# Performance work log

Measured on AMD Instinct MI355X. Metric: run time of the kernel, lower is better.

## Reference

```python
import jax, jax.numpy as jnp
import numpy as np

DZ, DA, K, T, BS, H = 32, 16, 3, 128, 512, 128


def setup_inputs() -> dict:
    key = jax.random.key(0)
    ks = jax.random.split(key, 8)
    s = 0.02
    # A/C: identity-like init (as in the torch module) plus small noise, per mixture k and timestep t
    A = jnp.eye(DZ, dtype=jnp.float32) + s * jax.random.normal(ks[0], (K, T, DZ, DZ), jnp.float32)
    C = jnp.eye(DA, DZ, dtype=jnp.float32) + s * jax.random.normal(ks[1], (K, T, DA, DZ), jnp.float32)
    a0 = jnp.zeros((DA,), jnp.float32)
    a = jax.random.normal(ks[2], (BS, T, DA), jnp.float32)

    def lw(k, shape):
        return 0.05 * jax.random.normal(k, shape, jnp.float32)

    Wih0 = lw(ks[3], (4 * H, DA)); Whh0 = lw(ks[4], (4 * H, H))
    bih0 = jnp.zeros((4 * H,), jnp.float32); bhh0 = jnp.zeros((4 * H,), jnp.float32)
    Wih1 = lw(ks[5], (4 * H, H)); Whh1 = lw(ks[6], (4 * H, H))
    bih1 = jnp.zeros((4 * H,), jnp.float32); bhh1 = jnp.zeros((4 * H,), jnp.float32)
    Wlin = lw(ks[7], (K, H)); blin = jnp.zeros((K,), jnp.float32)
    return dict(a=a, A=A, C=C, a0=a0, Wih0=Wih0, Whh0=Whh0, bih0=bih0, bhh0=bhh0,
                Wih1=Wih1, Whh1=Whh1, bih1=bih1, bhh1=bhh1, Wlin=Wlin, blin=blin)


def _lstm_layer(x, Wih, Whh, bih, bhh):
    # x: (bs, L, din) -> (bs, L, H); PyTorch gate order i, f, g, o; zero initial state
    Hd = Whh.shape[1]
    b = bih + bhh

    def step(carry, xt):
        h, c = carry
        g = xt @ Wih.T + h @ Whh.T + b
        i, f, gg, o = jnp.split(g, 4, axis=-1)
        c = jax.nn.sigmoid(f) * c + jax.nn.sigmoid(i) * jnp.tanh(gg)
        h = jax.nn.sigmoid(o) * jnp.tanh(c)
        return (h, c), h

    h0 = jnp.zeros((x.shape[0], Hd), x.dtype)
    _, hs = jax.lax.scan(step, (h0, h0), jnp.swapaxes(x, 0, 1))
    return jnp.swapaxes(hs, 0, 1)


def _filter(a, A, C, a0, Wih0, Whh0, bih0, bhh0, Wih1, Whh1, bih1, bhh1, Wlin, blin):
    bs, L, da = a.shape
    dz = A.shape[-1]
    R = 0.01 * jnp.eye(da, dtype=a.dtype)
    Q = 0.01 * jnp.eye(dz, dtype=a.dtype)

    # dynamics network: alpha_t from [a_0, a_0..a_{L-2}]
    code = jnp.concatenate([jnp.broadcast_to(a0, (bs, 1, da)), a[:, :-1]], axis=1)
    h = _lstm_layer(code, Wih0, Whh0, bih0, bhh0)
    h = _lstm_layer(h, Wih1, Whh1, bih1, bhh1)
    alpha = jax.nn.softmax(h @ Wlin.T + blin, axis=-1)  # (bs, L, K)

    A_mix = jnp.einsum('blk,klij->blij', alpha, A)  # (bs, L, dz, dz)
    C_mix = jnp.einsum('blk,klij->blij', alpha, C)  # (bs, L, da, dz)
    # A is applied at index t+1 for the prediction step; last slot is a dummy (its output is unused)
    A_next = jnp.concatenate([A_mix[:, 1:], A_mix[:, -1:]], axis=1)

    mu0 = jnp.zeros((bs, dz), a.dtype)
    sig0 = jnp.broadcast_to(jnp.eye(dz, dtype=a.dtype), (bs, dz, dz))
    I = jnp.eye(dz, dtype=a.dtype)

    def step(carry, inp):
        mu_pred, sigma_pred = carry
        Ct, At_next, at = inp  # (bs,da,dz), (bs,dz,dz), (bs,da)
        r = at - jnp.einsum('bij,bj->bi', Ct, mu_pred)
        CtT = jnp.swapaxes(Ct, 1, 2)
        S = Ct @ sigma_pred @ CtT + R                      # (bs, da, da)
        Kg = sigma_pred @ CtT @ jnp.linalg.inv(S)          # (bs, dz, da)
        mu = mu_pred + jnp.einsum('bij,bj->bi', Kg, r)
        sigma = (I - Kg @ Ct) @ sigma_pred
        mu_next = jnp.einsum('bij,bj->bi', At_next, mu)
        sigma_next = At_next @ sigma @ jnp.swapaxes(At_next, 1, 2) + Q
        return (mu_next, sigma_next), mu

    xs = (jnp.swapaxes(C_mix, 0, 1), jnp.swapaxes(A_next, 0, 1), jnp.swapaxes(a, 0, 1))
    _, means = jax.lax.scan(step, (mu0, sig0), xs)
    return jnp.swapaxes(means, 0, 1)  # filtered means (bs, L, dz)


def reference(a, A, C, a0, Wih0, Whh0, bih0, bhh0, Wih1, Whh1, bih1, bhh1, Wlin, blin):
    return _filter(a, A, C, a0, Wih0, Whh0, bih0, bhh0,
                   Wih1, Whh1, bih1, bhh1, Wlin, blin)
```

## Files before the change

kernel.cpp:

```cpp
#include <hip/hip_runtime.h>
#include <hip/hip_fp16.h>
#include <cstdint>

#define T_LEN 128
#define DA    16
#define DZ    32
#define HH    128

__device__ __forceinline__ float sigm(float x){ return 1.0f/(1.0f + __expf(-x)); }
__device__ __forceinline__ float tanh_f(float x){ return 1.0f - 2.0f/(__expf(2.0f*x)+1.0f); }
__device__ __forceinline__ float dot4(float4 a, float4 b){ return a.x*b.x + a.y*b.y + a.z*b.z + a.w*b.w; }

typedef _Float16 h2v __attribute__((ext_vector_type(2)));
__device__ __forceinline__ float fdot2(uint32_t w, uint32_t h, float acc){
  union{uint32_t u; h2v v;} a, b; a.u = w; b.u = h;
  return __builtin_amdgcn_fdot2(a.v, b.v, acc, false);
}
__device__ __forceinline__ uint32_t packh2(float x, float y){
  return (uint32_t)__half_as_ushort(__float2half(x)) |
         ((uint32_t)__half_as_ushort(__float2half(y)) << 16);
}

#define BAR() do { asm volatile("s_waitcnt lgkmcnt(0)" ::: "memory"); \
                   __builtin_amdgcn_s_barrier(); } while (0)


__global__ void prep_kernel(const float* __restrict__ Wih0, const float* __restrict__ Whh0,
                            const float* __restrict__ bih0, const float* __restrict__ bhh0,
                            const float* __restrict__ Wih1, const float* __restrict__ Whh1,
                            const float* __restrict__ bih1, const float* __restrict__ bhh1,
                            uint32_t* __restrict__ ws) {
  int idx = blockIdx.x*256 + threadIdx.x;
  if (idx < 4096) {
    int q = idx & 3, g = (idx >> 2) & 511, m = idx >> 11;
    int k0 = 8*m + 2*q;
    ws[idx] = packh2(Wih0[g*DA + k0], Wih0[g*DA + k0 + 1]);
  } else if (idx < 36864) {
    int f = idx - 4096;
    int q = f & 3, g = (f >> 2) & 511, m = f >> 11;
    int k0 = 8*m + 2*q;
    ws[idx] = packh2(Whh0[g*HH + k0], Whh0[g*HH + k0 + 1]);
  } else if (idx < 69632) {
    int f = idx - 36864;
    int q = f & 3, g = (f >> 2) & 511, m = f >> 11;
    int k0 = 8*m + 2*q;
    ws[idx] = packh2(Wih1[g*HH + k0], Wih1[g*HH + k0 + 1]);
  } else if (idx < 102400) {
    int f = idx - 69632;
    int q = f & 3, g = (f >> 2) & 511, m = f >> 11;
    int k0 = 8*m + 2*q;
    ws[idx] = packh2(Whh1[g*HH + k0], Whh1[g*HH + k0 + 1]);
  } else if (idx < 102912) {
    int j = idx - 102400;
    ((float*)ws)[idx] = bih0[j] + bhh0[j];
  } else if (idx < 103424) {
    int j = idx - 102912;
    ((float*)ws)[idx] = bih1[j] + bhh1[j];
  }
}

__global__ __launch_bounds__(512, 2) void lstm_kernel(
    const float* __restrict__ a, const float* __restrict__ a0,
    const uint32_t* __restrict__ wsw, const float* __restrict__ Wlin,
    const float* __restrict__ blin, float* __restrict__ alpha_out) {
  const uint4* Wih0p = (const uint4*)(wsw);
  const uint4* Whh0p = (const uint4*)(wsw + 4096);
  const uint4* Wih1p = (const uint4*)(wsw + 36864);
  const uint4* Whh1p = (const uint4*)(wsw + 69632);
  const float* b0v = (const float*)(wsw + 102400);
  const float* b1v = (const float*)(wsw + 102912);

  __shared__ __align__(16) uint32_t sxh[2][T_LEN][8];
  __shared__ __align__(16) uint32_t sh0h[2][64];
  __shared__ __align__(16) uint32_t sh1h[2][64];
  __shared__ float gates[2][4*HH];

  int tid = threadIdx.x;
  int lane = tid & 63;
  int wv = tid >> 6;
  int bb = blockIdx.x * 2;

  uint4 wi0[2], wh0[16], wi1[16], wh1[16];
  #pragma unroll
  for (int m = 0; m < 2; ++m)  wi0[m] = Wih0p[m*512 + tid];
  #pragma unroll
  for (int m = 0; m < 16; ++m) wh0[m] = Whh0p[m*512 + tid];
  #pragma unroll
  for (int m = 0; m < 16; ++m) wi1[m] = Wih1p[m*512 + tid];
  #pragma unroll
  for (int m = 0; m < 16; ++m) wh1[m] = Whh1p[m*512 + tid];
  float bi0 = b0v[tid], bi1 = b1v[tid];

  for (int i = tid; i < 2*T_LEN*8; i += 512) {
    int r = i / (T_LEN*8), rem = i % (T_LEN*8), t = rem >> 3, p = rem & 7;
    float x0, x1;
    if (t == 0) { x0 = a0[2*p]; x1 = a0[2*p+1]; }
    else {
      const float* src = a + ((size_t)(bb + r)*T_LEN + (t-1))*DA;
      x0 = src[2*p]; x1 = src[2*p+1];
    }
    sxh[r][t][p] = packh2(x0, x1);
  }
  float wl00 = Wlin[0*HH + 2*lane], wl01 = Wlin[0*HH + 2*lane+1];
  float wl10 = Wlin[1*HH + 2*lane], wl11 = Wlin[1*HH + 2*lane+1];
  float wl20 = Wlin[2*HH + 2*lane], wl21 = Wlin[2*HH + 2*lane+1];
  float bl0 = blin[0], bl1 = blin[1], bl2 = blin[2];
  float c00 = 0.f, c01 = 0.f, c10 = 0.f, c11 = 0.f;
  if (tid < 128) { sh0h[wv][lane] = 0u; sh1h[wv][lane] = 0u; }
  __syncthreads();

  #pragma unroll 1
  for (int t = 0; t < T_LEN; ++t) {
    {
      float g0a = bi0, g0b = 0.f, g1a = bi0, g1b = 0.f;
      uint4 xA0 = *(const uint4*)&sxh[0][t][0];
      uint4 xA1 = *(const uint4*)&sxh[0][t][4];
      uint4 xB0 = *(const uint4*)&sxh[1][t][0];
      uint4 xB1 = *(const uint4*)&sxh[1][t][4];
      g0a = fdot2(wi0[0].x, xA0.x, g0a); g0b = fdot2(wi0[0].y, xA0.y, g0b);
      g0a = fdot2(wi0[0].z, xA0.z, g0a); g0b = fdot2(wi0[0].w, xA0.w, g0b);
      g0a = fdot2(wi0[1].x, xA1.x, g0a); g0b = fdot2(wi0[1].y, xA1.y, g0b);
      g0a = fdot2(wi0[1].z, xA1.z, g0a); g0b = fdot2(wi0[1].w, xA1.w, g0b);
      g1a = fdot2(wi0[0].x, xB0.x, g1a); g1b = fdot2(wi0[0].y, xB0.y, g1b);
      g1a = fdot2(wi0[0].z, xB0.z, g1a); g1b = fdot2(wi0[0].w, xB0.w, g1b);
      g1a = fdot2(wi0[1].x, xB1.x, g1a); g1b = fdot2(wi0[1].y, xB1.y, g1b);
      g1a = fdot2(wi0[1].z, xB1.z, g1a); g1b = fdot2(wi0[1].w, xB1.w, g1b);
      #pragma unroll
      for (int m = 0; m < 16; ++m) {
        uint4 w = wh0[m];
        uint4 hA = *(const uint4*)&sh0h[0][4*m];
        uint4 hB = *(const uint4*)&sh0h[1][4*m];
        g0a = fdot2(w.x, hA.x, g0a); g0b = fdot2(w.y, hA.y, g0b);
        g0a = fdot2(w.z, hA.z, g0a); g0b = fdot2(w.w, hA.w, g0b);
        g1a = fdot2(w.x, hB.x, g1a); g1b = fdot2(w.y, hB.y, g1b);
        g1a = fdot2(w.z, hB.z, g1a); g1b = fdot2(w.w, hB.w, g1b);
      }
      gates[0][tid] = g0a + g0b;
      gates[1][tid] = g1a + g1b;
    }
    __syncthreads();
    if (tid < 128) {
      int j0 = 2*lane, j1 = j0 + 1;
      float i0 = gates[wv][j0],      f0 = gates[wv][j0+HH],
            q0 = gates[wv][j0+2*HH], o0 = gates[wv][j0+3*HH];
      c00 = sigm(f0)*c00 + sigm(i0)*tanh_f(q0);
      float hv0 = sigm(o0)*tanh_f(c00);
      float i1 = gates[wv][j1],      f1 = gates[wv][j1+HH],
            q1 = gates[wv][j1+2*HH], o1 = gates[wv][j1+3*HH];
      c01 = sigm(f1)*c01 + sigm(i1)*tanh_f(q1);
      float hv1 = sigm(o1)*tanh_f(c01);
      sh0h[wv][lane] = packh2(hv0, hv1);
    }
    __syncthreads();
    {
      float g0a = bi1, g0b = 0.f, g1a = bi1, g1b = 0.f;
      #pragma unroll
      for (int m = 0; m < 16; ++m) {
        uint4 w = wi1[m];
        uint4 hA = *(const uint4*)&sh0h[0][4*m];
        uint4 hB = *(const uint4*)&sh0h[1][4*m];
        g0a = fdot2(w.x, hA.x, g0a); g0b = fdot2(w.y, hA.y, g0b);
        g0a = fdot2(w.z, hA.z, g0a); g0b = fdot2(w.w, hA.w, g0b);
        g1a = fdot2(w.x, hB.x, g1a); g1b = fdot2(w.y, hB.y, g1b);
        g1a = fdot2(w.z, hB.z, g1a); g1b = fdot2(w.w, hB.w, g1b);
      }
      #pragma unroll
      for (int m = 0; m < 16; ++m) {
        uint4 w = wh1[m];
        uint4 hA = *(const uint4*)&sh1h[0][4*m];
        uint4 hB = *(const uint4*)&sh1h[1][4*m];
        g0a = fdot2(w.x, hA.x, g0a); g0b = fdot2(w.y, hA.y, g0b);
        g0a = fdot2(w.z, hA.z, g0a); g0b = fdot2(w.w, hA.w, g0b);
        g1a = fdot2(w.x, hB.x, g1a); g1b = fdot2(w.y, hB.y, g1b);
        g1a = fdot2(w.w, hB.w, g1b); g1a = fdot2(w.z, hB.z, g1a);
      }
      gates[0][tid] = g0a + g0b;
      gates[1][tid] = g1a + g1b;
    }
    __syncthreads();
    float hv0 = 0.f, hv1 = 0.f;
    if (tid < 128) {
      int j0 = 2*lane, j1 = j0 + 1;
      float i0 = gates[wv][j0],      f0 = gates[wv][j0+HH],
            q0 = gates[wv][j0+2*HH], o0 = gates[wv][j0+3*HH];
      c10 = sigm(f0)*c10 + sigm(i0)*tanh_f(q0);
      hv0 = sigm(o0)*tanh_f(c10);
      float i1 = gates[wv][j1],      f1 = gates[wv][j1+HH],
            q1 = gates[wv][j1+2*HH], o1 = gates[wv][j1+3*HH];
      c11 = sigm(f1)*c11 + sigm(i1)*tanh_f(q1);
      hv1 = sigm(o1)*tanh_f(c11);
      sh1h[wv][lane] = packh2(hv0, hv1);
    }
    __syncthreads();
    if (tid < 128) {
      float p0 = hv0*wl00 + hv1*wl01;
      float p1 = hv0*wl10 + hv1*wl11;
      float p2 = hv0*wl20 + hv1*wl21;
      #pragma unroll
      for (int off = 32; off > 0; off >>= 1) {
        p0 += __shfl_down(p0, off); p1 += __shfl_down(p1, off); p2 += __shfl_down(p2, off);
      }
      if (lane == 0) {
        float l0 = p0 + bl0, l1 = p1 + bl1, l2 = p2 + bl2;
        float mx = fmaxf(l0, fmaxf(l1, l2));
        float e0=__expf(l0-mx), e1=__expf(l1-mx), e2=__expf(l2-mx);
        float inv = 1.0f/(e0+e1+e2);
        float* dst = alpha_out + (((size_t)(bb+wv))*T_LEN + t)*3;
        dst[0]=e0*inv; dst[1]=e1*inv; dst[2]=e2*inv;
      }
    }
  }
}

__global__ __launch_bounds__(256) void kalman_kernel(
    const float* __restrict__ a, const float* __restrict__ A,
    const float* __restrict__ C, const float* __restrict__ alpha,
    float* __restrict__ out) {
  __shared__ __align__(16) float Sg[DZ][36];
  __shared__ __align__(16) float Am[DZ][36];
  __shared__ __align__(16) float AmT[DZ][36];
  __shared__ __align__(16) float Cm[DA][36];
  __shared__ __align__(16) float Nn[DZ][20];
  __shared__ __align__(16) float NnT[DA][36];
  __shared__ __align__(16) float Aug[DA][36];
  __shared__ __align__(16) float Kg[DZ][20];
  __shared__ __align__(16) float Sp2[DZ][36];
  __shared__ __align__(16) float T2m[DZ][36];
  __shared__ __align__(16) float sa[T_LEN][DA];
  __shared__ float salpha[T_LEN*3];
  __shared__ __align__(16) float muv[DZ], mun[DZ], rv[DA];

  int tid = threadIdx.x;
  int b = blockIdx.x;

  for (int e = tid; e < T_LEN*DA; e += 256) (&sa[0][0])[e] = a[(size_t)b*T_LEN*DA + e];
  for (int e = tid; e < T_LEN*3; e += 256) salpha[e] = alpha[(size_t)b*T_LEN*3 + e];
  for (int e = tid; e < DZ*36; e += 256) (&Sg[0][0])[e] = 0.0f;
  __syncthreads();
  if (tid < DZ) { Sg[tid][tid] = 1.0f; muv[tid] = 0.0f; }

  const int i8 = tid >> 3, jA = tid & 7, jB = jA + 8, j4m = jA * 4;
  const int i16 = tid >> 4, j16 = tid & 15;
  const int iR = tid & 31, j4r = (tid >> 5) * 4;

  const float4* A4 = (const float4*)A;
  const float4* C4 = (const float4*)C;
  float4 pA0 = A4[(0*T_LEN + 1)*256 + tid];
  float4 pA1 = A4[(1*T_LEN + 1)*256 + tid];
  float4 pA2 = A4[(2*T_LEN + 1)*256 + tid];
  float4 pC0, pC1, pC2;
  if (tid < 128) {
    pC0 = C4[(0*T_LEN + 0)*128 + tid];
    pC1 = C4[(1*T_LEN + 0)*128 + tid];
    pC2 = C4[(2*T_LEN + 0)*128 + tid];
  }
  __syncthreads();

  #pragma unroll 1
  for (int t = 0; t < T_LEN; ++t) {
    int ta = (t < T_LEN-1) ? t+1 : t;
    float b10 = salpha[ta*3+0], b11 = salpha[ta*3+1], b12 = salpha[ta*3+2];
    float b00 = salpha[t*3+0],  b01 = salpha[t*3+1],  b02 = salpha[t*3+2];

    {
      float4 v;
      v.x = b10*pA0.x + b11*pA1.x + b12*pA2.x;
      v.y = b10*pA0.y + b11*pA1.y + b12*pA2.y;
      v.z = b10*pA0.z + b11*pA1.z + b12*pA2.z;
      v.w = b10*pA0.w + b11*pA1.w + b12*pA2.w;
      *(float4*)&Am[i8][j4m] = v;
      AmT[j4m+0][i8] = v.x; AmT[j4m+1][i8] = v.y;
      AmT[j4m+2][i8] = v.z; AmT[j4m+3][i8] = v.w;
      if (tid < 128) {
        float4 c;
        c.x = b00*pC0.x + b01*pC1.x + b02*pC2.x;
        c.y = b00*pC0.y + b01*pC1.y + b02*pC2.y;
        c.z = b00*pC0.z + b01*pC1.z + b02*pC2.z;
        c.w = b00*pC0.w + b01*pC1.w + b02*pC2.w;
        *(float4*)&Cm[tid>>3][(tid&7)*4] = c;
      }
      int tn  = (t+1 < T_LEN) ? t+1 : T_LEN-1;
      int tan = (tn < T_LEN-1) ? tn+1 : tn;
      pA0 = A4[(0*T_LEN + tan)*256 + tid];
      pA1 = A4[(1*T_LEN + tan)*256 + tid];
      pA2 = A4[(2*T_LEN + tan)*256 + tid];
      if (tid < 128) {
        pC0 = C4[(0*T_LEN + tn)*128 + tid];
        pC1 = C4[(1*T_LEN + tn)*128 + tid];
        pC2 = C4[(2*T_LEN + tn)*128 + tid];
      }
    }
    BAR();

    {
      float accA = 0.0f, accB = 0.0f;
      #pragma unroll
      for (int k4 = 0; k4 < 8; ++k4) {
        float4 s  = *(const float4*)&Sg[i8][k4*4];
        float4 cA = *(const float4*)&Cm[jA][k4*4];
        float4 cB = *(const float4*)&Cm[jB][k4*4];
        accA += dot4(s,cA); accB += dot4(s,cB);
      }
      Nn[i8][jA] = accA; Nn[i8][jB] = accB;
      NnT[jA][i8] = accA; NnT[jB][i8] = accB;
      if (tid >= 192 && tid < 192 + DA) {
        int j = tid - 192;
        float acc = sa[t][j];
        #pragma unroll
        for (int k4 = 0; k4 < 8; ++k4)
          acc -= dot4(*(const float4*)&Cm[j][k4*4], *(const float4*)&muv[k4*4]);
        rv[j] = acc;
      }
    }
    BAR();

    {
      float acc = 0.0f;
      #pragma unroll
      for (int k4 = 0; k4 < 8; ++k4) {
        float4 c = *(const float4*)&Cm[i16][k4*4];
        float4 n = *(const float4*)&NnT[j16][k4*4];
        acc += dot4(c,n);
      }
      Aug[i16][j16] = acc + ((i16 == j16) ? 0.01f : 0.0f);
      Aug[i16][16 + j16] = (i16 == j16) ? 1.0f : 0.0f;
    }
    BAR();

    if (tid < 64) {
      int lane = tid;
      int r = lane >> 2, cb = lane & 3;
      float v[8];
      #pragma unroll
      for (int j = 0; j < 8; ++j) v[j] = Aug[r][cb*8 + j];
      #define GJ_PIVOT(P, CTRL)                                                \
      {                                                                        \
        float App = __int_as_float(__builtin_amdgcn_readlane(                  \
                      __float_as_int(v[(P) & 7]), ((P) << 2) | ((P) >> 3)));   \
        float fv  = __int_as_float(__builtin_amdgcn_mov_dpp(                   \
                      __float_as_int(v[(P) & 7]), (CTRL), 0xf, 0xf, true));    \
        float prow[8];                                                         \
        _Pragma("unroll")                                                      \
        for (int j = 0; j < 8; ++j) prow[j] = __shfl(v[j], ((P) << 2) | cb, 64); \
        float pinv = 1.0f / App;                                               \
        if (r == (P)) {                                                        \
          _Pragma("unroll")                                                    \
          for (int j = 0; j < 8; ++j) v[j] *= pinv;                            \
        } else {                                                               \
          float fp = fv * pinv;                                                \
          _Pragma("unroll")                                                    \
          for (int j = 0; j < 8; ++j) v[j] -= fp * prow[j];                    \
        }                                                                      \
      }
      GJ_PIVOT(0, 0x00)  GJ_PIVOT(1, 0x00)  GJ_PIVOT(2, 0x00)  GJ_PIVOT(3, 0x00)
      GJ_PIVOT(4, 0x00)  GJ_PIVOT(5, 0x00)  GJ_PIVOT(6, 0x00)  GJ_PIVOT(7, 0x00)
      GJ_PIVOT(8, 0x55)  GJ_PIVOT(9, 0x55)  GJ_PIVOT(10, 0x55) GJ_PIVOT(11, 0x55)
      GJ_PIVOT(12, 0x55) GJ_PIVOT(13, 0x55) GJ_PIVOT(14, 0x55) GJ_PIVOT(15, 0x55)
      #undef GJ_PIVOT
      if (cb >= 2) {
        #pragma unroll
        for (int j = 0; j < 8; ++j) Aug[r][cb*8 + j] = v[j];
      }
    }
    BAR();

    {
      float accA = 0.0f, accB = 0.0f;
      #pragma unroll
      for (int k4 = 0; k4 < 4; ++k4) {
        float4 n  = *(const float4*)&Nn[i8][k4*4];
        float4 sA = *(const float4*)&Aug[jA][16 + k4*4];
        float4 sB = *(const float4*)&Aug[jB][16 + k4*4];
        accA += dot4(n,sA); accB += dot4(n,sB);
      }
      Kg[i8][jA] = accA; Kg[i8][jB] = accB;
    }
    BAR();

    if (tid >= 64 && tid < 64 + DZ) {
      int j = tid - 64;
      float m = muv[j];
      #pragma unroll
      for (int k4 = 0; k4 < 4; ++k4)
        m += dot4(*(const float4*)&Kg[j][k4*4], *(const float4*)&rv[k4*4]);
      mun[j] = m;
      out[((size_t)b*T_LEN + t)*DZ + j] = m;
    }
    {
      float4 acc = *(const float4*)&Sg[iR][j4r];
      #pragma unroll
      for (int k4 = 0; k4 < 4; ++k4) {
        float4 kv = *(const float4*)&Kg[iR][k4*4];
        float4 n0 = *(const float4*)&NnT[4*k4+0][j4r];
        float4 n1 = *(const float4*)&NnT[4*k4+1][j4r];
        float4 n2 = *(const float4*)&NnT[4*k4+2][j4r];
        float4 n3 = *(const float4*)&NnT[4*k4+3][j4r];
        acc.x -= kv.x*n0.x + kv.y*n1.x + kv.z*n2.x + kv.w*n3.x;
        acc.y -= kv.x*n0.y + kv.y*n1.y + kv.z*n2.y + kv.w*n3.y;
        acc.z -= kv.x*n0.z + kv.y*n1.z + kv.z*n2.z + kv.w*n3.z;
        acc.w -= kv.x*n0.w + kv.y*n1.w + kv.z*n2.w + kv.w*n3.w;
      }
      *(float4*)&Sp2[iR][j4r] = acc;
    }
    BAR();

    {
      float4 acc = make_float4(0.f,0.f,0.f,0.f);
      #pragma unroll
      for (int k4 = 0; k4 < 8; ++k4) {
        float4 av = *(const float4*)&Am[iR][k4*4];
        float4 b0 = *(const float4*)&Sp2[4*k4+0][j4r];
        float4 b1 = *(const float4*)&Sp2[4*k4+1][j4r];
        float4 b2 = *(const float4*)&Sp2[4*k4+2][j4r];
        float4 b3 = *(const float4*)&Sp2[4*k4+3][j4r];
        acc.x += av.x*b0.x + av.y*b1.x + av.z*b2.x + av.w*b3.x;
        acc.y += av.x*b0.y + av.y*b1.y + av.z*b2.y + av.w*b3.y;
        acc.z += av.x*b0.z + av.y*b1.z + av.z*b2.z + av.w*b3.z;
        acc.w += av.x*b0.w + av.y*b1.w + av.z*b2.w + av.w*b3.w;
      }
      *(float4*)&T2m[iR][j4r] = acc;
    }
    BAR();

    {
      float4 acc = make_float4(0.f,0.f,0.f,0.f);
      #pragma unroll
      for (int k4 = 0; k4 < 8; ++k4) {
        float4 tv = *(const float4*)&T2m[iR][k4*4];
        float4 b0 = *(const float4*)&AmT[4*k4+0][j4r];
        float4 b1 = *(const float4*)&AmT[4*k4+1][j4r];
        float4 b2 = *(const float4*)&AmT[4*k4+2][j4r];
        float4 b3 = *(const float4*)&AmT[4*k4+3][j4r];
        acc.x += tv.x*b0.x + tv.y*b1.x + tv.z*b2.x + tv.w*b3.x;
        acc.y += tv.x*b0.y + tv.y*b1.y + tv.z*b2.y + tv.w*b3.y;
        acc.z += tv.x*b0.z + tv.y*b1.z + tv.z*b2.z + tv.w*b3.z;
        acc.w += tv.x*b0.w + tv.y*b1.w + tv.z*b2.w + tv.w*b3.w;
      }
      int d = iR - j4r;
      if (d >= 0 && d < 4) (&acc.x)[d] += 0.01f;
      *(float4*)&Sg[iR][j4r] = acc;
    }
    if (tid >= 128 && tid < 128 + DZ) {
      int j = tid - 128;
      float m = 0.0f;
      #pragma unroll
      for (int k4 = 0; k4 < 8; ++k4)
        m += dot4(*(const float4*)&Am[j][k4*4], *(const float4*)&mun[k4*4]);
      muv[j] = m;
    }
    BAR();
  }
}

extern "C" void kernel_launch(void* const* d_in, const int* in_sizes, int n_in,
                              void* d_out, int out_size, void* d_ws, size_t ws_size,
                              hipStream_t stream) {
  const float* a    = (const float*)d_in[0];
  const float* A    = (const float*)d_in[1];
  const float* C    = (const float*)d_in[2];
  const float* a0   = (const float*)d_in[3];
  const float* Wih0 = (const float*)d_in[4];
  const float* Whh0 = (const float*)d_in[5];
  const float* bih0 = (const float*)d_in[6];
  const float* bhh0 = (const float*)d_in[7];
  const float* Wih1 = (const float*)d_in[8];
  const float* Whh1 = (const float*)d_in[9];
  const float* bih1 = (const float*)d_in[10];
  const float* bhh1 = (const float*)d_in[11];
  const float* Wlin = (const float*)d_in[12];
  const float* blin = (const float*)d_in[13];
  uint32_t* ws = (uint32_t*)d_ws;
  float* alpha = (float*)(ws + 103424);
  float* out = (float*)d_out;

  prep_kernel<<<404, 256, 0, stream>>>(Wih0, Whh0, bih0, bhh0, Wih1, Whh1, bih1, bhh1, ws);
  lstm_kernel<<<256, 512, 0, stream>>>(a, a0, ws, Wlin, blin, alpha);
  kalman_kernel<<<512, 256, 0, stream>>>(a, A, C, alpha, out);
}
```

Before: 1.247 ms.

## Restructure Kalman matmuls to exploit symmetry and drop transposed shared copies

Rewrites the per-step Kalman matrix products so each thread keeps a row of the left operand in registers and dots it with rows of the right operand. This relies on the symmetry of Sigma, N and Sp2, which removes the transposed AmT and NnT shared-memory copies and their strided stores. Work is concentrated on 64 or 128 threads with more outputs per thread, and the mean update is merged into the covariance-update phase. A malformed fdot2 accumulation in the LSTM layer-1 loop is also corrected, which changes numerics there.

```diff
diff --git a/kernel.cpp b/kernel.cpp
--- a/kernel.cpp
+++ b/kernel.cpp
@@ -172,7 +172,7 @@
         g0a = fdot2(w.x, hA.x, g0a); g0b = fdot2(w.y, hA.y, g0b);
         g0a = fdot2(w.z, hA.z, g0a); g0b = fdot2(w.w, hA.w, g0b);
         g1a = fdot2(w.x, hB.x, g1a); g1b = fdot2(w.y, hB.y, g1b);
-        g1a = fdot2(w.w, hB.w, g1b); g1a = fdot2(w.z, hB.z, g1a);
+        g1a = fdot2(w.z, hB.z, g1a); g1b = fdot2(w.w, hB.w, g1b);
       }
       gates[0][tid] = g0a + g0b;
       gates[1][tid] = g1a + g1b;
@@ -218,10 +218,8 @@
     float* __restrict__ out) {
   __shared__ __align__(16) float Sg[DZ][36];
   __shared__ __align__(16) float Am[DZ][36];
-  __shared__ __align__(16) float AmT[DZ][36];
   __shared__ __align__(16) float Cm[DA][36];
   __shared__ __align__(16) float Nn[DZ][20];
-  __shared__ __align__(16) float NnT[DA][36];
   __shared__ __align__(16) float Aug[DA][36];
   __shared__ __align__(16) float Kg[DZ][20];
   __shared__ __align__(16) float Sp2[DZ][36];
@@ -239,9 +237,10 @@
   __syncthreads();
   if (tid < DZ) { Sg[tid][tid] = 1.0f; muv[tid] = 0.0f; }
 
-  const int i8 = tid >> 3, jA = tid & 7, jB = jA + 8, j4m = jA * 4;
-  const int i16 = tid >> 4, j16 = tid & 15;
-  const int iR = tid & 31, j4r = (tid >> 5) * 4;
+  const int i8 = tid >> 3, j4m = (tid & 7) * 4;
+  const int i32 = tid & 31;
+  const int s8  = (tid >> 5) * 8;
+  const int s4  = (tid >> 5) * 4;
 
   const float4* A4 = (const float4*)A;
   const float4* C4 = (const float4*)C;
@@ -269,8 +268,6 @@
       v.z = b10*pA0.z + b11*pA1.z + b12*pA2.z;
       v.w = b10*pA0.w + b11*pA1.w + b12*pA2.w;
       *(float4*)&Am[i8][j4m] = v;
-      AmT[j4m+0][i8] = v.x; AmT[j4m+1][i8] = v.y;
-      AmT[j4m+2][i8] = v.z; AmT[j4m+3][i8] = v.w;
       if (tid < 128) {
         float4 c;
         c.x = b00*pC0.x + b01*pC1.x + b02*pC2.x;
@@ -292,38 +289,56 @@
     }
     BAR();
 
-    {
-      float accA = 0.0f, accB = 0.0f;
+    if (tid < 64) {
+      float4 sg[8];
+      #pragma unroll
+      for (int k4 = 0; k4 < 8; ++k4) sg[k4] = *(const float4*)&Sg[i32][4*k4];
+      float acc[8];
+      #pragma unroll
+      for (int c = 0; c < 8; ++c) {
+        float d = 0.f;
+        #pragma unroll
+        for (int k4 = 0; k4 < 8; ++k4)
+          d += dot4(sg[k4], *(const float4*)&Cm[s8+c][4*k4]);
+        acc[c] = d;
+      }
+      *(float4*)&Nn[i32][s8]   = make_float4(acc[0],acc[1],acc[2],acc[3]);
+      *(float4*)&Nn[i32][s8+4] = make_float4(acc[4],acc[5],acc[6],acc[7]);
+    } else if (tid >= 192 && tid < 192 + DA) {
+      int j = tid - 192;
+      float acc = sa[t][j];
+      #pragma unroll
+      for (int k4 = 0; k4 < 8; ++k4)
+        acc -= dot4(*(const float4*)&Cm[j][4*k4], *(const float4*)&muv[4*k4]);
+      rv[j] = acc;
+    }
+    BAR();
+
+    if (tid < 64) {
+      int i = tid & 15, j4 = (tid >> 4) * 4;
+      float4 cm[8];
+      #pragma unroll
+      for (int k4 = 0; k4 < 8; ++k4) cm[k4] = *(const float4*)&Cm[i][4*k4];
+      float4 acc = make_float4(0.f,0.f,0.f,0.f);
       #pragma unroll
       for (int k4 = 0; k4 < 8; ++k4) {
-        float4 s  = *(const float4*)&Sg[i8][k4*4];
-        float4 cA = *(const float4*)&Cm[jA][k4*4];
-        float4 cB = *(const float4*)&Cm[jB][k4*4];
-        accA += dot4(s,cA); accB += dot4(s,cB);
-      }
-      Nn[i8][jA] = accA; Nn[i8][jB] = accB;
-      NnT[jA][i8] = accA; NnT[jB][i8] = accB;
-      if (tid >= 192 && tid < 192 + DA) {
-        int j = tid - 192;
-        float acc = sa[t][j];
-        #pragma unroll
-        for (int k4 = 0; k4 < 8; ++k4)
-          acc -= dot4(*(const float4*)&Cm[j][k4*4], *(const float4*)&muv[k4*4]);
-        rv[j] = acc;
-      }
-    }
-    BAR();
-
-    {
-      float acc = 0.0f;
-      #pragma unroll
-      for (int k4 = 0; k4 < 8; ++k4) {
-        float4 c = *(const float4*)&Cm[i16][k4*4];
-        float4 n = *(const float4*)&NnT[j16][k4*4];
-        acc += dot4(c,n);
-      }
-      Aug[i16][j16] = acc + ((i16 == j16) ? 0.01f : 0.0f);
-      Aug[i16][16 + j16] = (i16 == j16) ? 1.0f : 0.0f;
+        float4 n0 = *(const float4*)&Nn[4*k4+0][j4];
+        float4 n1 = *(const float4*)&Nn[4*k4+1][j4];
+        float4 n2 = *(const float4*)&Nn[4*k4+2][j4];
+        float4 n3 = *(const float4*)&Nn[4*k4+3][j4];
+        acc.x += cm[k4].x*n0.x + cm[k4].y*n1.x + cm[k4].z*n2.x + cm[k4].w*n3.x;
+        acc.y += cm[k4].x*n0.y + cm[k4].y*n1.y + cm[k4].z*n2.y + cm[k4].w*n3.y;
+        acc.z += cm[k4].x*n0.z + cm[k4].y*n1.z + cm[k4].z*n2.z + cm[k4].w*n3.z;
+        acc.w += cm[k4].x*n0.w + cm[k4].y*n1.w + cm[k4].z*n2.w + cm[k4].w*n3.w;
+      }
+      acc.x += (i == j4+0) ? 0.01f : 0.f;
+      acc.y += (i == j4+1) ? 0.01f : 0.f;
+      acc.z += (i == j4+2) ? 0.01f : 0.f;
+      acc.w += (i == j4+3) ? 0.01f : 0.f;
+      *(float4*)&Aug[i][j4] = acc;
+      *(float4*)&Aug[i][16+j4] = make_float4(
+          (i==j4+0)?1.f:0.f, (i==j4+1)?1.f:0.f,
+          (i==j4+2)?1.f:0.f, (i==j4+3)?1.f:0.f);
     }
     BAR();
 
@@ -364,88 +379,93 @@
     }
     BAR();
 
-    {
-      float accA = 0.0f, accB = 0.0f;
-      #pragma unroll
-      for (int k4 = 0; k4 < 4; ++k4) {
-        float4 n  = *(const float4*)&Nn[i8][k4*4];
-        float4 sA = *(const float4*)&Aug[jA][16 + k4*4];
-        float4 sB = *(const float4*)&Aug[jB][16 + k4*4];
-        accA += dot4(n,sA); accB += dot4(n,sB);
-      }
-      Kg[i8][jA] = accA; Kg[i8][jB] = accB;
-    }
-    BAR();
-
-    if (tid >= 64 && tid < 64 + DZ) {
-      int j = tid - 64;
+    if (tid < 128) {
+      float4 nn[4];
+      #pragma unroll
+      for (int k4 = 0; k4 < 4; ++k4) nn[k4] = *(const float4*)&Nn[i32][4*k4];
+      float acc[4];
+      #pragma unroll
+      for (int c = 0; c < 4; ++c) {
+        float d = 0.f;
+        #pragma unroll
+        for (int k4 = 0; k4 < 4; ++k4)
+          d += dot4(nn[k4], *(const float4*)&Aug[s4+c][16+4*k4]);
+        acc[c] = d;
+      }
+      *(float4*)&Kg[i32][s4] = make_float4(acc[0],acc[1],acc[2],acc[3]);
+    }
+    BAR();
+
+    if (tid < 128) {
+      float4 kg[4];
+      #pragma unroll
+      for (int k4 = 0; k4 < 4; ++k4) kg[k4] = *(const float4*)&Kg[i32][4*k4];
+      float4 sg0 = *(const float4*)&Sg[i32][s8];
+      float4 sg1 = *(const float4*)&Sg[i32][s8+4];
+      float acc[8];
+      #pragma unroll
+      for (int c = 0; c < 8; ++c) {
+        float d = 0.f;
+        #pragma unroll
+        for (int k4 = 0; k4 < 4; ++k4)
+          d += dot4(kg[k4], *(const float4*)&Nn[s8+c][4*k4]);
+        acc[c] = d;
+      }
+      *(float4*)&Sp2[i32][s8] =
+          make_float4(sg0.x-acc[0], sg0.y-acc[1], sg0.z-acc[2], sg0.w-acc[3]);
+      *(float4*)&Sp2[i32][s8+4] =
+          make_float4(sg1.x-acc[4], sg1.y-acc[5], sg1.z-acc[6], sg1.w-acc[7]);
+    } else if (tid < 128 + DZ) {
+      int j = tid - 128;
       float m = muv[j];
       #pragma unroll
       for (int k4 = 0; k4 < 4; ++k4)
-        m += dot4(*(const float4*)&Kg[j][k4*4], *(const float4*)&rv[k4*4]);
+        m += dot4(*(const float4*)&Kg[j][4*k4], *(const float4*)&rv[4*k4]);
       mun[j] = m;
       out[((size_t)b*T_LEN + t)*DZ + j] = m;
     }
-    {
-      float4 acc = *(const float4*)&Sg[iR][j4r];
-      #pragma unroll
-      for (int k4 = 0; k4 < 4; ++k4) {
-        float4 kv = *(const float4*)&Kg[iR][k4*4];
-        float4 n0 = *(const float4*)&NnT[4*k4+0][j4r];
-        float4 n1 = *(const float4*)&NnT[4*k4+1][j4r];
-        float4 n2 = *(const float4*)&NnT[4*k4+2][j4r];
-        float4 n3 = *(const float4*)&NnT[4*k4+3][j4r];
-        acc.x -= kv.x*n0.x + kv.y*n1.x + kv.z*n2.x + kv.w*n3.x;
-        acc.y -= kv.x*n0.y + kv.y*n1.y + kv.z*n2.y + kv.w*n3.y;
-        acc.z -= kv.x*n0.z + kv.y*n1.z + kv.z*n2.z + kv.w*n3.z;
-        acc.w -= kv.x*n0.w + kv.y*n1.w + kv.z*n2.w + kv.w*n3.w;
-      }
-      *(float4*)&Sp2[iR][j4r] = acc;
-    }
-    BAR();
-
-    {
-      float4 acc = make_float4(0.f,0.f,0.f,0.f);
-      #pragma unroll
-      for (int k4 = 0; k4 < 8; ++k4) {
-        float4 av = *(const float4*)&Am[iR][k4*4];
-        float4 b0 = *(const float4*)&Sp2[4*k4+0][j4r];
-        float4 b1 = *(const float4*)&Sp2[4*k4+1][j4r];
-        float4 b2 = *(const float4*)&Sp2[4*k4+2][j4r];
-        float4 b3 = *(const float4*)&Sp2[4*k4+3][j4r];
-        acc.x += av.x*b0.x + av.y*b1.x + av.z*b2.x + av.w*b3.x;
-        acc.y += av.x*b0.y + av.y*b1.y + av.z*b2.y + av.w*b3.y;
-        acc.z += av.x*b0.z + av.y*b1.z + av.z*b2.z + av.w*b3.z;
-        acc.w += av.x*b0.w + av.y*b1.w + av.z*b2.w + av.w*b3.w;
-      }
-      *(float4*)&T2m[iR][j4r] = acc;
-    }
-    BAR();
-
-    {
-      float4 acc = make_float4(0.f,0.f,0.f,0.f);
-      #pragma unroll
-      for (int k4 = 0; k4 < 8; ++k4) {
-        float4 tv = *(const float4*)&T2m[iR][k4*4];
-        float4 b0 = *(const float4*)&AmT[4*k4+0][j4r];
-        float4 b1 = *(const float4*)&AmT[4*k4+1][j4r];
-        float4 b2 = *(const float4*)&AmT[4*k4+2][j4r];
-        float4 b3 = *(const float4*)&AmT[4*k4+3][j4r];
-        acc.x += tv.x*b0.x + tv.y*b1.x + tv.z*b2.x + tv.w*b3.x;
-        acc.y += tv.x*b0.y + tv.y*b1.y + tv.z*b2.y + tv.w*b3.y;
-        acc.z += tv.x*b0.z + tv.y*b1.z + tv.z*b2.z + tv.w*b3.z;
-        acc.w += tv.x*b0.w + tv.y*b1.w + tv.z*b2.w + tv.w*b3.w;
-      }
-      int d = iR - j4r;
-      if (d >= 0 && d < 4) (&acc.x)[d] += 0.01f;
-      *(float4*)&Sg[iR][j4r] = acc;
-    }
-    if (tid >= 128 && tid < 128 + DZ) {
+    BAR();
+
+    if (tid < 128) {
+      float4 am[8];
+      #pragma unroll
+      for (int k4 = 0; k4 < 8; ++k4) am[k4] = *(const float4*)&Am[i32][4*k4];
+      float acc[8];
+      #pragma unroll
+      for (int c = 0; c < 8; ++c) {
+        float d = 0.f;
+        #pragma unroll
+        for (int k4 = 0; k4 < 8; ++k4)
+          d += dot4(am[k4], *(const float4*)&Sp2[s8+c][4*k4]);
+        acc[c] = d;
+      }
+      *(float4*)&T2m[i32][s8]   = make_float4(acc[0],acc[1],acc[2],acc[3]);
+      *(float4*)&T2m[i32][s8+4] = make_float4(acc[4],acc[5],acc[6],acc[7]);
+    }
+    BAR();
+
+    if (tid < 128) {
+      float4 t2[8];
+      #pragma unroll
+      for (int k4 = 0; k4 < 8; ++k4) t2[k4] = *(const float4*)&T2m[i32][4*k4];
+      float acc[8];
+      #pragma unroll
+      for (int c = 0; c < 8; ++c) {
+        float d = 0.f;
+        #pragma unroll
+        for (int k4 = 0; k4 < 8; ++k4)
+          d += dot4(t2[k4], *(const float4*)&Am[s8+c][4*k4]);
+        if (i32 == s8+c) d += 0.01f;
+        acc[c] = d;
+      }
+      *(float4*)&Sg[i32][s8]   = make_float4(acc[0],acc[1],acc[2],acc[3]);
+      *(float4*)&Sg[i32][s8+4] = make_float4(acc[4],acc[5],acc[6],acc[7]);
+    } else if (tid < 128 + DZ) {
       int j = tid - 128;
       float m = 0.0f;
       #pragma unroll
       for (int k4 = 0; k4 < 8; ++k4)
-        m += dot4(*(const float4*)&Am[j][k4*4], *(const float4*)&mun[k4*4]);
+        m += dot4(*(const float4*)&Am[j][4*k4], *(const float4*)&mun[4*k4]);
       muv[j] = m;
     }
     BAR();
```

New measurement: 1.523 ms. +22.1%, slower.

## Store Kalman covariance matrices in fp16 and use packed dot2 instructions

Applied to the files above, without the earlier changes.

Converts the Kalman filter's shared-memory matrices (covariance, A, C, intermediate products, gain, S inverse) from fp32 to packed fp16. The matmuls now use v_dot2 fp16 instructions with fp32 accumulation, and the stages are reorganized: the residual computation moves into the Gauss-Jordan phase and the transposed-A buffer is removed. The goal is fewer LDS bytes and fewer ALU ops per step on the serial time loop. The risk is that the covariance precision drops to fp16 across 128 recursive steps. The diff also fixes a mis-ordered accumulator in the LSTM layer-1 loop.

```diff
diff --git a/kernel.cpp b/kernel.cpp
--- a/kernel.cpp
+++ b/kernel.cpp
@@ -20,10 +20,25 @@
   return (uint32_t)__half_as_ushort(__float2half(x)) |
          ((uint32_t)__half_as_ushort(__float2half(y)) << 16);
 }
+__device__ __forceinline__ float h2lo(uint32_t u){
+  return __half2float(__ushort_as_half((unsigned short)(u & 0xffffu)));
+}
+__device__ __forceinline__ float h2hi(uint32_t u){
+  return __half2float(__ushort_as_half((unsigned short)(u >> 16)));
+}
+__device__ __forceinline__ float dot8(uint4 a, uint4 b, float acc){
+  acc = fdot2(a.x, b.x, acc); acc = fdot2(a.y, b.y, acc);
+  acc = fdot2(a.z, b.z, acc); acc = fdot2(a.w, b.w, acc);
+  return acc;
+}
+__device__ __forceinline__ float dot8f(uint4 h, float4 f0, float4 f1, float acc){
+  acc += h2lo(h.x)*f0.x + h2hi(h.x)*f0.y + h2lo(h.y)*f0.z + h2hi(h.y)*f0.w;
+  acc += h2lo(h.z)*f1.x + h2hi(h.z)*f1.y + h2lo(h.w)*f1.z + h2hi(h.w)*f1.w;
+  return acc;
+}
 
 #define BAR() do { asm volatile("s_waitcnt lgkmcnt(0)" ::: "memory"); \
                    __builtin_amdgcn_s_barrier(); } while (0)
-
 
 __global__ void prep_kernel(const float* __restrict__ Wih0, const float* __restrict__ Whh0,
                             const float* __restrict__ bih0, const float* __restrict__ bhh0,
@@ -172,7 +187,7 @@
         g0a = fdot2(w.x, hA.x, g0a); g0b = fdot2(w.y, hA.y, g0b);
         g0a = fdot2(w.z, hA.z, g0a); g0b = fdot2(w.w, hA.w, g0b);
         g1a = fdot2(w.x, hB.x, g1a); g1b = fdot2(w.y, hB.y, g1b);
-        g1a = fdot2(w.w, hB.w, g1b); g1a = fdot2(w.z, hB.z, g1a);
+        g1a = fdot2(w.z, hB.z, g1a); g1b = fdot2(w.w, hB.w, g1b);
       }
       gates[0][tid] = g0a + g0b;
       gates[1][tid] = g1a + g1b;
@@ -216,32 +231,38 @@
     const float* __restrict__ a, const float* __restrict__ A,
     const float* __restrict__ C, const float* __restrict__ alpha,
     float* __restrict__ out) {
-  __shared__ __align__(16) float Sg[DZ][36];
-  __shared__ __align__(16) float Am[DZ][36];
-  __shared__ __align__(16) float AmT[DZ][36];
-  __shared__ __align__(16) float Cm[DA][36];
-  __shared__ __align__(16) float Nn[DZ][20];
-  __shared__ __align__(16) float NnT[DA][36];
+  __shared__ __align__(16) uint32_t SgH[DZ][20];
+  __shared__ __align__(16) uint32_t AmH[DZ][20];
+  __shared__ __align__(16) uint32_t Sp2H[DZ][20];
+  __shared__ __align__(16) uint32_t T2H[DZ][20];
+  __shared__ __align__(16) uint32_t CmH[DA][20];
+  __shared__ __align__(16) uint32_t NnTH[DA][20];
+  __shared__ __align__(16) uint32_t NnH[DZ][12];
+  __shared__ __align__(16) uint32_t KgH[DZ][12];
+  __shared__ __align__(16) uint32_t SinvH[DA][12];
   __shared__ __align__(16) float Aug[DA][36];
-  __shared__ __align__(16) float Kg[DZ][20];
-  __shared__ __align__(16) float Sp2[DZ][36];
-  __shared__ __align__(16) float T2m[DZ][36];
   __shared__ __align__(16) float sa[T_LEN][DA];
   __shared__ float salpha[T_LEN*3];
-  __shared__ __align__(16) float muv[DZ], mun[DZ], rv[DA];
+  __shared__ __align__(16) float muvF[DZ], munF[DZ], rv[DA];
 
   int tid = threadIdx.x;
   int b = blockIdx.x;
 
   for (int e = tid; e < T_LEN*DA; e += 256) (&sa[0][0])[e] = a[(size_t)b*T_LEN*DA + e];
   for (int e = tid; e < T_LEN*3; e += 256) salpha[e] = alpha[(size_t)b*T_LEN*3 + e];
-  for (int e = tid; e < DZ*36; e += 256) (&Sg[0][0])[e] = 0.0f;
   __syncthreads();
-  if (tid < DZ) { Sg[tid][tid] = 1.0f; muv[tid] = 0.0f; }
-
-  const int i8 = tid >> 3, jA = tid & 7, jB = jA + 8, j4m = jA * 4;
-  const int i16 = tid >> 4, j16 = tid & 15;
-  const int iR = tid & 31, j4r = (tid >> 5) * 4;
+
+  const int i8 = tid >> 3, jq = tid & 7;
+  const int i32 = tid & 31, g = tid >> 5;
+  const int j2 = g * 2, j4 = g * 4;
+
+  {
+    uint2 iv;
+    iv.x = packh2((i8==4*jq  )?1.f:0.f, (i8==4*jq+1)?1.f:0.f);
+    iv.y = packh2((i8==4*jq+2)?1.f:0.f, (i8==4*jq+3)?1.f:0.f);
+    *(uint2*)&SgH[i8][jq*2] = iv;
+    if (tid < DZ) muvF[tid] = 0.0f;
+  }
 
   const float4* A4 = (const float4*)A;
   const float4* C4 = (const float4*)C;
@@ -263,21 +284,19 @@
     float b00 = salpha[t*3+0],  b01 = salpha[t*3+1],  b02 = salpha[t*3+2];
 
     {
-      float4 v;
-      v.x = b10*pA0.x + b11*pA1.x + b12*pA2.x;
-      v.y = b10*pA0.y + b11*pA1.y + b12*pA2.y;
-      v.z = b10*pA0.z + b11*pA1.z + b12*pA2.z;
-      v.w = b10*pA0.w + b11*pA1.w + b12*pA2.w;
-      *(float4*)&Am[i8][j4m] = v;
-      AmT[j4m+0][i8] = v.x; AmT[j4m+1][i8] = v.y;
-      AmT[j4m+2][i8] = v.z; AmT[j4m+3][i8] = v.w;
+      float vx = b10*pA0.x + b11*pA1.x + b12*pA2.x;
+      float vy = b10*pA0.y + b11*pA1.y + b12*pA2.y;
+      float vz = b10*pA0.z + b11*pA1.z + b12*pA2.z;
+      float vw = b10*pA0.w + b11*pA1.w + b12*pA2.w;
+      uint2 pv; pv.x = packh2(vx, vy); pv.y = packh2(vz, vw);
+      *(uint2*)&AmH[i8][jq*2] = pv;
       if (tid < 128) {
-        float4 c;
-        c.x = b00*pC0.x + b01*pC1.x + b02*pC2.x;
-        c.y = b00*pC0.y + b01*pC1.y + b02*pC2.y;
-        c.z = b00*pC0.z + b01*pC1.z + b02*pC2.z;
-        c.w = b00*pC0.w + b01*pC1.w + b02*pC2.w;
-        *(float4*)&Cm[tid>>3][(tid&7)*4] = c;
+        float cx = b00*pC0.x + b01*pC1.x + b02*pC2.x;
+        float cy = b00*pC0.y + b01*pC1.y + b02*pC2.y;
+        float cz = b00*pC0.z + b01*pC1.z + b02*pC2.z;
+        float cw = b00*pC0.w + b01*pC1.w + b02*pC2.w;
+        uint2 pc; pc.x = packh2(cx, cy); pc.y = packh2(cz, cw);
+        *(uint2*)&CmH[tid>>3][(tid&7)*2] = pc;
       }
       int tn  = (t+1 < T_LEN) ? t+1 : T_LEN-1;
       int tan = (tn < T_LEN-1) ? tn+1 : tn;
@@ -293,37 +312,40 @@
     BAR();
 
     {
-      float accA = 0.0f, accB = 0.0f;
-      #pragma unroll
-      for (int k4 = 0; k4 < 8; ++k4) {
-        float4 s  = *(const float4*)&Sg[i8][k4*4];
-        float4 cA = *(const float4*)&Cm[jA][k4*4];
-        float4 cB = *(const float4*)&Cm[jB][k4*4];
-        accA += dot4(s,cA); accB += dot4(s,cB);
-      }
-      Nn[i8][jA] = accA; Nn[i8][jB] = accB;
-      NnT[jA][i8] = accA; NnT[jB][i8] = accB;
-      if (tid >= 192 && tid < 192 + DA) {
-        int j = tid - 192;
-        float acc = sa[t][j];
-        #pragma unroll
-        for (int k4 = 0; k4 < 8; ++k4)
-          acc -= dot4(*(const float4*)&Cm[j][k4*4], *(const float4*)&muv[k4*4]);
-        rv[j] = acc;
-      }
-    }
-    BAR();
-
-    {
-      float acc = 0.0f;
-      #pragma unroll
-      for (int k4 = 0; k4 < 8; ++k4) {
-        float4 c = *(const float4*)&Cm[i16][k4*4];
-        float4 n = *(const float4*)&NnT[j16][k4*4];
-        acc += dot4(c,n);
-      }
-      Aug[i16][j16] = acc + ((i16 == j16) ? 0.01f : 0.0f);
-      Aug[i16][16 + j16] = (i16 == j16) ? 1.0f : 0.0f;
+      uint4 s0 = *(const uint4*)&SgH[i32][0];
+      uint4 s1 = *(const uint4*)&SgH[i32][4];
+      uint4 s2 = *(const uint4*)&SgH[i32][8];
+      uint4 s3 = *(const uint4*)&SgH[i32][12];
+      uint4 cA0 = *(const uint4*)&CmH[j2][0];
+      uint4 cA1 = *(const uint4*)&CmH[j2][4];
+      uint4 cA2 = *(const uint4*)&CmH[j2][8];
+      uint4 cA3 = *(const uint4*)&CmH[j2][12];
+      uint4 cB0 = *(const uint4*)&CmH[j2+1][0];
+      uint4 cB1 = *(const uint4*)&CmH[j2+1][4];
+      uint4 cB2 = *(const uint4*)&CmH[j2+1][8];
+      uint4 cB3 = *(const uint4*)&CmH[j2+1][12];
+      float aA = dot8(s3,cA3, dot8(s2,cA2, dot8(s1,cA1, dot8(s0,cA0, 0.f))));
+      float aB = dot8(s3,cB3, dot8(s2,cB2, dot8(s1,cB1, dot8(s0,cB0, 0.f))));
+      NnH[i32][g] = packh2(aA, aB);
+      __half* ntp = (__half*)&NnTH[0][0];
+      ntp[j2*40 + i32]     = __float2half(aA);
+      ntp[(j2+1)*40 + i32] = __float2half(aB);
+    }
+    BAR();
+
+    {
+      int i = tid & 15, j = tid >> 4;
+      uint4 c0 = *(const uint4*)&CmH[i][0];
+      uint4 c1 = *(const uint4*)&CmH[i][4];
+      uint4 c2 = *(const uint4*)&CmH[i][8];
+      uint4 c3 = *(const uint4*)&CmH[i][12];
+      uint4 n0 = *(const uint4*)&NnTH[j][0];
+      uint4 n1 = *(const uint4*)&NnTH[j][4];
+      uint4 n2 = *(const uint4*)&NnTH[j][8];
+      uint4 n3 = *(const uint4*)&NnTH[j][12];
+      float s = dot8(c3,n3, dot8(c2,n2, dot8(c1,n1, dot8(c0,n0, 0.f))));
+      Aug[i][j] = s + ((i == j) ? 0.01f : 0.0f);
+      Aug[i][16 + j] = (i == j) ? 1.0f : 0.0f;
     }
     BAR();
 
@@ -358,95 +380,124 @@
       GJ_PIVOT(12, 0x55) GJ_PIVOT(13, 0x55) GJ_PIVOT(14, 0x55) GJ_PIVOT(15, 0x55)
       #undef GJ_PIVOT
       if (cb >= 2) {
-        #pragma unroll
-        for (int j = 0; j < 8; ++j) Aug[r][cb*8 + j] = v[j];
-      }
-    }
-    BAR();
-
-    {
-      float accA = 0.0f, accB = 0.0f;
-      #pragma unroll
-      for (int k4 = 0; k4 < 4; ++k4) {
-        float4 n  = *(const float4*)&Nn[i8][k4*4];
-        float4 sA = *(const float4*)&Aug[jA][16 + k4*4];
-        float4 sB = *(const float4*)&Aug[jB][16 + k4*4];
-        accA += dot4(n,sA); accB += dot4(n,sB);
-      }
-      Kg[i8][jA] = accA; Kg[i8][jB] = accB;
-    }
-    BAR();
-
-    if (tid >= 64 && tid < 64 + DZ) {
+        uint4 w;
+        w.x = packh2(v[0], v[1]); w.y = packh2(v[2], v[3]);
+        w.z = packh2(v[4], v[5]); w.w = packh2(v[6], v[7]);
+        *(uint4*)&SinvH[r][(cb-2)*4] = w;
+      }
+    } else if (tid < 64 + DA) {
       int j = tid - 64;
-      float m = muv[j];
-      #pragma unroll
-      for (int k4 = 0; k4 < 4; ++k4)
-        m += dot4(*(const float4*)&Kg[j][k4*4], *(const float4*)&rv[k4*4]);
-      mun[j] = m;
-      out[((size_t)b*T_LEN + t)*DZ + j] = m;
-    }
-    {
-      float4 acc = *(const float4*)&Sg[iR][j4r];
-      #pragma unroll
-      for (int k4 = 0; k4 < 4; ++k4) {
-        float4 kv = *(const float4*)&Kg[iR][k4*4];
-        float4 n0 = *(const float4*)&NnT[4*k4+0][j4r];
-        float4 n1 = *(const float4*)&NnT[4*k4+1][j4r];
-        float4 n2 = *(const float4*)&NnT[4*k4+2][j4r];
-        float4 n3 = *(const float4*)&NnT[4*k4+3][j4r];
-        acc.x -= kv.x*n0.x + kv.y*n1.x + kv.z*n2.x + kv.w*n3.x;
-        acc.y -= kv.x*n0.y + kv.y*n1.y + kv.z*n2.y + kv.w*n3.y;
-        acc.z -= kv.x*n0.z + kv.y*n1.z + kv.z*n2.z + kv.w*n3.z;
-        acc.w -= kv.x*n0.w + kv.y*n1.w + kv.z*n2.w + kv.w*n3.w;
-      }
-      *(float4*)&Sp2[iR][j4r] = acc;
-    }
-    BAR();
-
-    {
-      float4 acc = make_float4(0.f,0.f,0.f,0.f);
-      #pragma unroll
-      for (int k4 = 0; k4 < 8; ++k4) {
-        float4 av = *(const float4*)&Am[iR][k4*4];
-        float4 b0 = *(const float4*)&Sp2[4*k4+0][j4r];
-        float4 b1 = *(const float4*)&Sp2[4*k4+1][j4r];
-        float4 b2 = *(const float4*)&Sp2[4*k4+2][j4r];
-        float4 b3 = *(const float4*)&Sp2[4*k4+3][j4r];
-        acc.x += av.x*b0.x + av.y*b1.x + av.z*b2.x + av.w*b3.x;
-        acc.y += av.x*b0.y + av.y*b1.y + av.z*b2.y + av.w*b3.y;
-        acc.z += av.x*b0.z + av.y*b1.z + av.z*b2.z + av.w*b3.z;
-        acc.w += av.x*b0.w + av.y*b1.w + av.z*b2.w + av.w*b3.w;
-      }
-      *(float4*)&T2m[iR][j4r] = acc;
-    }
-    BAR();
-
-    {
-      float4 acc = make_float4(0.f,0.f,0.f,0.f);
-      #pragma unroll
-      for (int k4 = 0; k4 < 8; ++k4) {
-        float4 tv = *(const float4*)&T2m[iR][k4*4];
-        float4 b0 = *(const float4*)&AmT[4*k4+0][j4r];
-        float4 b1 = *(const float4*)&AmT[4*k4+1][j4r];
-        float4 b2 = *(const float4*)&AmT[4*k4+2][j4r];
-        float4 b3 = *(const float4*)&AmT[4*k4+3][j4r];
-        acc.x += tv.x*b0.x + tv.y*b1.x + tv.z*b2.x + tv.w*b3.x;
-        acc.y += tv.x*b0.y + tv.y*b1.y + tv.z*b2.y + tv.w*b3.y;
-        acc.z += tv.x*b0.z + tv.y*b1.z + tv.z*b2.z + tv.w*b3.z;
-        acc.w += tv.x*b0.w + tv.y*b1.w + tv.z*b2.w + tv.w*b3.w;
-      }
-      int d = iR - j4r;
-      if (d >= 0 && d < 4) (&acc.x)[d] += 0.01f;
-      *(float4*)&Sg[iR][j4r] = acc;
+      uint4 c0 = *(const uint4*)&CmH[j][0];
+      uint4 c1 = *(const uint4*)&CmH[j][4];
+      uint4 c2 = *(const uint4*)&CmH[j][8];
+      uint4 c3 = *(const uint4*)&CmH[j][12];
+      const float4* mv = (const float4*)muvF;
+      float4 m0 = mv[0], m1 = mv[1], m2 = mv[2], m3 = mv[3];
+      float4 m4 = mv[4], m5 = mv[5], m6 = mv[6], m7 = mv[7];
+      float d = 0.f;
+      d = dot8f(c0, m0, m1, d);
+      d = dot8f(c1, m2, m3, d);
+      d = dot8f(c2, m4, m5, d);
+      d = dot8f(c3, m6, m7, d);
+      rv[j] = sa[t][j] - d;
+    }
+    BAR();
+
+    {
+      uint4 n0 = *(const uint4*)&NnH[i32][0];
+      uint4 n1 = *(const uint4*)&NnH[i32][4];
+      uint4 sA0 = *(const uint4*)&SinvH[j2][0];
+      uint4 sA1 = *(const uint4*)&SinvH[j2][4];
+      uint4 sB0 = *(const uint4*)&SinvH[j2+1][0];
+      uint4 sB1 = *(const uint4*)&SinvH[j2+1][4];
+      float aA = dot8(n1, sA1, dot8(n0, sA0, 0.f));
+      float aB = dot8(n1, sB1, dot8(n0, sB0, 0.f));
+      KgH[i32][g] = packh2(aA, aB);
+    }
+    BAR();
+
+    {
+      uint4 k0 = *(const uint4*)&KgH[i32][0];
+      uint4 k1 = *(const uint4*)&KgH[i32][4];
+      float acc[4];
+      #pragma unroll
+      for (int c = 0; c < 4; ++c) {
+        uint4 b0 = *(const uint4*)&NnH[j4+c][0];
+        uint4 b1 = *(const uint4*)&NnH[j4+c][4];
+        acc[c] = dot8(k1, b1, dot8(k0, b0, 0.f));
+      }
+      uint2 sgp = *(const uint2*)&SgH[i32][g*2];
+      uint2 o;
+      o.x = packh2(h2lo(sgp.x) - acc[0], h2hi(sgp.x) - acc[1]);
+      o.y = packh2(h2lo(sgp.y) - acc[2], h2hi(sgp.y) - acc[3]);
+      *(uint2*)&Sp2H[i32][g*2] = o;
     }
     if (tid >= 128 && tid < 128 + DZ) {
-      int j = tid - 128;
-      float m = 0.0f;
-      #pragma unroll
-      for (int k4 = 0; k4 < 8; ++k4)
-        m += dot4(*(const float4*)&Am[j][k4*4], *(const float4*)&mun[k4*4]);
-      muv[j] = m;
+      int q = tid - 128;
+      uint4 k0 = *(const uint4*)&KgH[q][0];
+      uint4 k1 = *(const uint4*)&KgH[q][4];
+      const float4* rp = (const float4*)rv;
+      float4 r0 = rp[0], r1 = rp[1], r2 = rp[2], r3 = rp[3];
+      float m = muvF[q];
+      m = dot8f(k0, r0, r1, m);
+      m = dot8f(k1, r2, r3, m);
+      munF[q] = m;
+      out[((size_t)b*T_LEN + t)*DZ + q] = m;
+    }
+    BAR();
+
+    {
+      uint4 a0 = *(const uint4*)&AmH[i32][0];
+      uint4 a1 = *(const uint4*)&AmH[i32][4];
+      uint4 a2 = *(const uint4*)&AmH[i32][8];
+      uint4 a3 = *(const uint4*)&AmH[i32][12];
+      float acc[4];
+      #pragma unroll
+      for (int c = 0; c < 4; ++c) {
+        uint4 p0 = *(const uint4*)&Sp2H[j4+c][0];
+        uint4 p1 = *(const uint4*)&Sp2H[j4+c][4];
+        uint4 p2 = *(const uint4*)&Sp2H[j4+c][8];
+        uint4 p3 = *(const uint4*)&Sp2H[j4+c][12];
+        acc[c] = dot8(a3,p3, dot8(a2,p2, dot8(a1,p1, dot8(a0,p0, 0.f))));
+      }
+      uint2 o; o.x = packh2(acc[0], acc[1]); o.y = packh2(acc[2], acc[3]);
+      *(uint2*)&T2H[i32][g*2] = o;
+    }
+    BAR();
+
+    {
+      uint4 t0 = *(const uint4*)&T2H[i32][0];
+      uint4 t1 = *(const uint4*)&T2H[i32][4];
+      uint4 t2 = *(const uint4*)&T2H[i32][8];
+      uint4 t3 = *(const uint4*)&T2H[i32][12];
+      float acc[4];
+      #pragma unroll
+      for (int c = 0; c < 4; ++c) {
+        uint4 a0 = *(const uint4*)&AmH[j4+c][0];
+        uint4 a1 = *(const uint4*)&AmH[j4+c][4];
+        uint4 a2 = *(const uint4*)&AmH[j4+c][8];
+        uint4 a3 = *(const uint4*)&AmH[j4+c][12];
+        acc[c] = dot8(t3,a3, dot8(t2,a2, dot8(t1,a1, dot8(t0,a0, 0.f))));
+        if (i32 == j4 + c) acc[c] += 0.01f;
+      }
+      uint2 o; o.x = packh2(acc[0], acc[1]); o.y = packh2(acc[2], acc[3]);
+      *(uint2*)&SgH[i32][g*2] = o;
+    }
+    if (tid >= 128 && tid < 128 + DZ) {
+      int q = tid - 128;
+      uint4 a0 = *(const uint4*)&AmH[q][0];
+      uint4 a1 = *(const uint4*)&AmH[q][4];
+      uint4 a2 = *(const uint4*)&AmH[q][8];
+      uint4 a3 = *(const uint4*)&AmH[q][12];
+      const float4* mp = (const float4*)munF;
+      float4 n0 = mp[0], n1 = mp[1], n2 = mp[2], n3 = mp[3];
+      float4 n4 = mp[4], n5 = mp[5], n6 = mp[6], n7 = mp[7];
+      float m = 0.f;
+      m = dot8f(a0, n0, n1, m);
+      m = dot8f(a1, n2, n3, m);
+      m = dot8f(a2, n4, n5, m);
+      m = dot8f(a3, n6, n7, m);
+      muvF[q] = m;
     }
     BAR();
   }
```

New measurement: 1.094 ms. -12.3%, faster.
